# Kernel optimization log

Measured on AMD Instinct MI355X. Metric: run time of the kernel, lower is better.

Reference implementation:

```python
import jax, jax.numpy as jnp
import numpy as np
import math
from jax import lax

B, V, C, G, D, H, W = 1, 5, 32, 8, 32, 192, 192
ATTN_TEMP = 1.0
SPLIT_ITV = 1.0


def _bilinear_sample(im, x, y):
    # im: [B,C,Hs,Ws]; x,y: [B,N] pixel coords. Matches F.grid_sample
    # (bilinear, padding_mode='zeros', align_corners=True).
    Bb, Cc, Hs, Ws = im.shape
    imf = im.reshape(Bb, Cc, Hs * Ws)
    x0 = jnp.floor(x)
    y0 = jnp.floor(y)
    wx = x - x0
    wy = y - y0

    def tap(ix, iy, w):
        inb = ((ix >= 0) & (ix <= Ws - 1) & (iy >= 0) & (iy <= Hs - 1)).astype(im.dtype)
        flat = (jnp.clip(iy, 0, Hs - 1) * Ws + jnp.clip(ix, 0, Ws - 1)).astype(jnp.int32)
        v = jnp.take_along_axis(imf, flat[:, None, :], axis=2)  # [B,C,N]
        return v * (w * inb)[:, None, :]

    return (tap(x0, y0, (1 - wx) * (1 - wy)) + tap(x0 + 1, y0, wx * (1 - wy))
            + tap(x0, y0 + 1, (1 - wx) * wy) + tap(x0 + 1, y0 + 1, wx * wy))


def _homo_warping(src_fea, src_proj, ref_proj, depth_values):
    Bb, Cc, Hs, Ws = src_fea.shape
    _, Dd, Hr, Wr = depth_values.shape
    proj = jnp.matmul(src_proj, jnp.linalg.inv(ref_proj))
    rot, trans = proj[:, :3, :3], proj[:, :3, 3:4]
    yy, xx = jnp.meshgrid(jnp.arange(Hr, dtype=jnp.float32),
                          jnp.arange(Wr, dtype=jnp.float32), indexing='ij')
    xyz = jnp.stack([xx.ravel(), yy.ravel(), jnp.ones(Hr * Wr, jnp.float32)])  # [3,N]
    rot_xyz = jnp.einsum('bij,jn->bin', rot, xyz)  # [B,3,N]
    proj_xyz = rot_xyz[:, :, None, :] * depth_values.reshape(Bb, 1, Dd, Hr * Wr) \
        + trans[:, :, None, :]  # [B,3,D,N]
    z = proj_xyz[:, 2]
    z = jnp.where(z == 0, 1e-9, z)
    # grid is built under torch.no_grad in the original -> stop_gradient
    px = lax.stop_gradient(proj_xyz[:, 0] / z)  # [B,D,N] pixel coords
    py = lax.stop_gradient(proj_xyz[:, 1] / z)
    samp = _bilinear_sample(src_fea, px.reshape(Bb, -1), py.reshape(Bb, -1))  # [B,C,D*N]
    warped = samp.reshape(Bb, Cc, Dd, Hr, Wr)
    valid = lax.stop_gradient((warped[:, 0] != 0).astype(src_fea.dtype))  # [B,D,H,W]
    return warped, valid


def _forward(ref_feature, src_features, rotation, normal_plane, proj_matrices,
             depth_hypo, w_reg, w_norm):
    nsrc = src_features.shape[0]
    ref_proj = proj_matrices[:, 0]
    inv_refR = jnp.linalg.inv(rotation[:, 0])
    ref_proj_new = ref_proj[:, 0].at[:, :3, :4].set(
        jnp.matmul(ref_proj[:, 1, :3, :3], ref_proj[:, 0, :3, :4]))
    ref_vol = ref_feature.reshape(B, G, C // G, 1, H, W)  # broadcast over D

    cor_feats = jnp.zeros((B, G, D, H, W), ref_feature.dtype)
    cor_weight_sum = jnp.full((B, D, H, W), 1e-8, ref_feature.dtype)
    sum_weight = jnp.full((B, G, D, H, W), 1e-8, ref_feature.dtype)
    sims = []
    num_valid = jnp.zeros((B, D, H, W), ref_feature.dtype)

    for i in range(nsrc):  # fixed small number of source views
        src_fea = src_features[i]
        src_proj = proj_matrices[:, i + 1]
        norv = jnp.matmul(rotation[:, i + 1], inv_refR)[:, 2, :]  # [B,3]
        # stage_idx = 1: avg_pool2d(k=1,s=1) is identity -> relu(.) + 0.01
        src_w = jax.nn.relu(jnp.einsum('bchw,bc->bhw', normal_plane, norv)) + 0.01
        src_proj_new = src_proj[:, 0].at[:, :3, :4].set(
            jnp.matmul(src_proj[:, 1, :3, :3], src_proj[:, 0, :3, :4]))
        warped, valid = _homo_warping(src_fea, src_proj_new, ref_proj_new, depth_hypo)
        num_valid = valid + num_valid
        sw_d = src_w[:, None] * valid  # [B,D,H,W]
        sims.append(sw_d.mean(axis=1))
        sw5 = sw_d[:, None]  # [B,1,D,H,W] broadcast over G (repeat in torch)
        sum_weight = sum_weight + sw5
        # group-wise correlation: group_cor=True
        cor_feat = (warped.reshape(B, G, C // G, D, H, W) * ref_vol).mean(axis=2)
        cor_w = jax.nn.softmax(cor_feat.sum(axis=1) / ATTN_TEMP, axis=1) / math.sqrt(C)
        cor_weight_sum = cor_weight_sum + cor_w
        cor_feats = cor_feats + cor_w[:, None] * (sw5 * cor_feat)

    cor_feats = cor_feats / sum_weight / cor_weight_sum[:, None]
    sum_weight = sum_weight / nsrc

    hmin = depth_hypo.min(axis=(1, 2, 3), keepdims=True)
    hmax = depth_hypo.max(axis=(1, 2, 3), keepdims=True)
    norm_hypo = lax.stop_gradient((depth_hypo - hmin) / (hmax - hmin))

    # regnet stand-in: per-group linear reduction + normalized-hypo bias
    attn_logits = jnp.einsum('bgdhw,g->bdhw', cor_feats, w_reg) + norm_hypo
    attn_weight = jax.nn.softmax(attn_logits, axis=1)
    # normalnet stand-in: 1x1 linear on the 3 normal channels
    est_normal_plane = jnp.einsum('bchw,oc->bohw', normal_plane, w_norm)

    idx = jnp.argmax(attn_weight, axis=1, keepdims=True)
    depth = jnp.take_along_axis(depth_hypo, idx, axis=1)[:, 0]  # [B,H,W]
    photometric_confidence = lax.stop_gradient(attn_weight.max(axis=1))
    weight = jnp.stack(sims)[None]  # [1,nsrc,B,H,W]

    last_itv = depth_hypo[:, 1] - depth_hypo[:, 0]
    min_depth = depth - SPLIT_ITV * last_itv
    max_depth = depth + SPLIT_ITV * last_itv
    return (depth, photometric_confidence, attn_weight, est_normal_plane,
            sum_weight[:, 0, 0], weight, num_valid, min_depth, max_depth)


def setup_inputs() -> dict:
    key = jax.random.key(0)
    ks = jax.random.split(key, 5)
    ref_feature = jax.random.normal(ks[0], (B, C, H, W), jnp.float32)
    src_features = jax.random.normal(ks[1], (V - 1, B, C, H, W), jnp.float32)
    normal_plane = jax.random.normal(ks[2], (B, 3, H, W), jnp.float32)
    w_reg = jax.random.normal(ks[3], (G,), jnp.float32) * 0.1
    w_norm = jax.random.normal(ks[4], (3, 3), jnp.float32) * 0.1
    # Small per-view rotations (about z and y) and translations; intrinsics K.
    rots, projs = [], []
    Kmat = np.eye(4, dtype=np.float32)
    Kmat[0, 0] = Kmat[1, 1] = 192.0
    Kmat[0, 2] = Kmat[1, 2] = 96.0
    for v in range(V):
        az, ay = 0.04 * v, 0.02 * v
        Rz = np.array([[np.cos(az), -np.sin(az), 0], [np.sin(az), np.cos(az), 0], [0, 0, 1]], np.float32)
        Ry = np.array([[np.cos(ay), 0, np.sin(ay)], [0, 1, 0], [-np.sin(ay), 0, np.cos(ay)]], np.float32)
        Rv = (Rz @ Ry).astype(np.float32)
        rots.append(Rv)
        E = np.eye(4, dtype=np.float32)
        E[:3, :3] = Rv
        E[0, 3] = 0.1 * v
        E[2, 3] = 0.02 * v
        projs.append(np.stack([E, Kmat]))
    rotation = jnp.asarray(np.stack(rots)[None])          # [1,V,3,3]
    proj_matrices = jnp.asarray(np.stack(projs)[None])    # [1,V,2,4,4]
    depth_hypo = jnp.broadcast_to(
        jnp.linspace(425.0, 935.0, D, dtype=jnp.float32).reshape(1, D, 1, 1),
        (B, D, H, W))
    return {"ref_feature": ref_feature, "src_features": src_features,
            "rotation": rotation, "normal_plane": normal_plane,
            "proj_matrices": proj_matrices, "depth_hypo": depth_hypo,
            "w_reg": w_reg, "w_norm": w_norm}


def reference(ref_feature, src_features, rotation, normal_plane, proj_matrices,
              depth_hypo, w_reg, w_norm):
    return _forward(ref_feature, src_features, rotation, normal_plane,
                    proj_matrices, depth_hypo, w_reg, w_norm)
```

## Files before the change

### kernel.cpp

```cpp
#include <hip/hip_runtime.h>
#include <math.h>

#define Vc 5
#define Cc 32
#define Gc 8
#define Dc 32
#define Hc 192
#define Wc 192
#define HWc (Hc*Wc)
#define NSRC (Vc-1)
#define NTILE (HWc/64)

#define OFF_DEPTH  0
#define OFF_CONF   (HWc)
#define OFF_ATTN   (2*HWc)
#define OFF_EST    (OFF_ATTN + Dc*HWc)
#define OFF_SW     (OFF_EST + 3*HWc)
#define OFF_WEIGHT (OFF_SW + HWc)
#define OFF_NVAL   (OFF_WEIGHT + NSRC*HWc)
#define OFF_MIN    (OFF_NVAL + Dc*HWc)
#define OFF_MAX    (OFF_MIN + HWc)

#define T_OFF 64
#define PART_OFF (T_OFF + 6*Cc*HWc)
#define NP_OFF (PART_OFF + 2*NTILE)

__device__ void inv4(const float* A, float* out) {
    float M[4][8];
    for (int r = 0; r < 4; r++) {
        for (int c = 0; c < 4; c++) { M[r][c] = A[r*4+c]; M[r][c+4] = (r == c) ? 1.f : 0.f; }
    }
    for (int col = 0; col < 4; col++) {
        int piv = col; float best = fabsf(M[col][col]);
        for (int r = col+1; r < 4; r++) { float v = fabsf(M[r][col]); if (v > best) { best = v; piv = r; } }
        if (piv != col) for (int c = 0; c < 8; c++) { float t = M[col][c]; M[col][c] = M[piv][c]; M[piv][c] = t; }
        float inv = 1.f / M[col][col];
        for (int c = 0; c < 8; c++) M[col][c] *= inv;
        for (int r = 0; r < 4; r++) {
            if (r == col) continue;
            float f = M[r][col];
            for (int c = 0; c < 8; c++) M[r][c] -= f * M[col][c];
        }
    }
    for (int r = 0; r < 4; r++) for (int c = 0; c < 4; c++) out[r*4+c] = M[r][c+4];
}

__device__ void inv3(const float* A, float* out) {
    float a=A[0],b=A[1],c=A[2],d=A[3],e=A[4],f=A[5],g=A[6],h=A[7],i=A[8];
    float det = a*(e*i-f*h) - b*(d*i-f*g) + c*(d*h-e*g);
    float id = 1.f/det;
    out[0]=(e*i-f*h)*id; out[1]=(c*h-b*i)*id; out[2]=(b*f-c*e)*id;
    out[3]=(f*g-d*i)*id; out[4]=(a*i-c*g)*id; out[5]=(c*d-a*f)*id;
    out[6]=(d*h-e*g)*id; out[7]=(b*g-a*h)*id; out[8]=(a*e-b*d)*id;
}

__device__ void setup_body(const float* __restrict__ rotation,
                           const float* __restrict__ proj,
                           float* __restrict__ wsf) {
    float refE[16], refK[16], refNew[16], invRef[16];
    for (int k = 0; k < 16; k++) { refE[k] = proj[k]; refK[k] = proj[16+k]; }
    for (int k = 0; k < 16; k++) refNew[k] = refE[k];
    for (int r = 0; r < 3; r++) for (int c = 0; c < 4; c++) {
        float s = 0.f;
        for (int k = 0; k < 3; k++) s += refK[r*4+k] * refE[k*4+c];
        refNew[r*4+c] = s;
    }
    inv4(refNew, invRef);
    float invR0[9];
    inv3(rotation, invR0);

    for (int i = 0; i < NSRC; i++) {
        const float* E = proj + (i+1)*32;
        const float* K = proj + (i+1)*32 + 16;
        float sNew[16];
        for (int k = 0; k < 16; k++) sNew[k] = E[k];
        for (int r = 0; r < 3; r++) for (int c = 0; c < 4; c++) {
            float s = 0.f;
            for (int k = 0; k < 3; k++) s += K[r*4+k] * E[k*4+c];
            sNew[r*4+c] = s;
        }
        float P[16];
        for (int r = 0; r < 4; r++) for (int c = 0; c < 4; c++) {
            float s = 0.f;
            for (int k = 0; k < 4; k++) s += sNew[r*4+k] * invRef[k*4+c];
            P[r*4+c] = s;
        }
        float* o = wsf + 2 + i*15;
        for (int r = 0; r < 3; r++) for (int c = 0; c < 3; c++) o[r*3+c] = P[r*4+c];
        for (int r = 0; r < 3; r++) o[9+r] = P[r*4+3];
        const float* Ri = rotation + (i+1)*9;
        for (int c = 0; c < 3; c++) {
            float s = 0.f;
            for (int k = 0; k < 3; k++) s += Ri[2*3+k] * invR0[k*3+c];
            o[12+c] = s;
        }
    }
}

__global__ __launch_bounds__(256)
void prep_kernel(const float* __restrict__ src,
                 const float* __restrict__ ref,
                 const float* __restrict__ depth,
                 const float* __restrict__ normal,
                 const float* __restrict__ rotation,
                 const float* __restrict__ proj,
                 float* __restrict__ wsf) {
    const int img = blockIdx.y;
    const int p0  = blockIdx.x * 64;
    const int t = threadIdx.x;

    if (img == 6) {
        __shared__ float tl[3][64];
        if (t < 192) { const int c = t >> 6, p = t & 63; tl[c][p] = normal[c*HWc + p0 + p]; }
        __syncthreads();
        const int p = t >> 2, c = t & 3;
        wsf[NP_OFF + (size_t)(p0 + p)*4 + c] = (c < 3) ? tl[c][p] : 0.f;
        return;
    }

    const float* in = (img < NSRC) ? (src + (size_t)img*Cc*HWc)
                    : (img == NSRC) ? ref : depth;
    float* outp = wsf + T_OFF + (size_t)img * Cc * HWc;
    __shared__ float tile[Cc][64+1];
    float mn = __uint_as_float(0x7F800000u);
    float mx = 0.f;
#pragma unroll
    for (int k = 0; k < 8; k++) {
        const int c = (t >> 6) + k*4;
        const int p = t & 63;
        const float v = in[(size_t)c*HWc + p0 + p];
        tile[c][p] = v;
        mn = fminf(mn, v);
        mx = fmaxf(mx, v);
    }
    __syncthreads();
#pragma unroll
    for (int k = 0; k < 8; k++) {
        const int c = t & 31;
        const int p = (t >> 5) + k*8;
        outp[(size_t)(p0 + p)*Cc + c] = tile[c][p];
    }
    if (img == 5) {
        for (int off = 32; off; off >>= 1) {
            mn = fminf(mn, __shfl_xor(mn, off));
            mx = fmaxf(mx, __shfl_xor(mx, off));
        }
        __shared__ float smn[4], smx[4];
        const int w = t >> 6;
        if ((t & 63) == 0) { smn[w] = mn; smx[w] = mx; }
        __syncthreads();
        if (t == 0) {
            for (int i = 1; i < 4; i++) { mn = fminf(mn, smn[i]); mx = fmaxf(mx, smx[i]); }
            wsf[PART_OFF + blockIdx.x*2 + 0] = mn;
            wsf[PART_OFF + blockIdx.x*2 + 1] = mx;
        }
    }
    if (img == 0 && blockIdx.x == 0 && t == 0)
        setup_body(rotation, proj, wsf);
}

__device__ __forceinline__ void compute_wo(float fxp, float fyp, const float* __restrict__ Wv,
                                           float dep, float4* wout, int4* oout) {
    const float b0 = Wv[0]*fxp + Wv[1]*fyp + Wv[2];
    const float b1 = Wv[3]*fxp + Wv[4]*fyp + Wv[5];
    const float b2 = Wv[6]*fxp + Wv[7]*fyp + Wv[8];
    float z = fmaf(b2, dep, Wv[11]);
    if (z == 0.f) z = 1e-9f;
    float rz = __builtin_amdgcn_rcpf(z);
    rz = rz * (2.f - z * rz);
    const float px = fmaf(b0, dep, Wv[9])  * rz;
    const float py = fmaf(b1, dep, Wv[10]) * rz;

    const float fx0 = floorf(px), fy0 = floorf(py);
    const float wx = px - fx0, wy = py - fy0;
    const float fx1 = fx0 + 1.f, fy1 = fy0 + 1.f;
    const bool ix0 = (fx0 >= 0.f) && (fx0 <= (float)(Wc-1));
    const bool ix1 = (fx1 >= 0.f) && (fx1 <= (float)(Wc-1));
    const bool iy0 = (fy0 >= 0.f) && (fy0 <= (float)(Hc-1));
    const bool iy1 = (fy1 >= 0.f) && (fy1 <= (float)(Hc-1));
    const float w00 = (1.f-wx)*(1.f-wy) * ((ix0 && iy0) ? 1.f : 0.f);
    const float w10 = wx*(1.f-wy)       * ((ix1 && iy0) ? 1.f : 0.f);
    const float w01 = (1.f-wx)*wy       * ((ix0 && iy1) ? 1.f : 0.f);
    const float w11 = wx*wy             * ((ix1 && iy1) ? 1.f : 0.f);
    const int xi0 = (int)fminf(fmaxf(fx0, 0.f), (float)(Wc-1));
    const int xi1 = (int)fminf(fmaxf(fx1, 0.f), (float)(Wc-1));
    const int yi0 = (int)fminf(fmaxf(fy0, 0.f), (float)(Hc-1));
    const int yi1 = (int)fminf(fmaxf(fy1, 0.f), (float)(Hc-1));
    *wout = make_float4(w00, w10, w01, w11);
    *oout = make_int4((yi0*Wc + xi0) << 7, (yi0*Wc + xi1) << 7,
                      (yi1*Wc + xi0) << 7, (yi1*Wc + xi1) << 7);
}

template<bool USE_NPT>
__global__ __launch_bounds__(128, 8)
void main_kernel_t(const float* __restrict__ normal_plane,
                   const float* __restrict__ w_reg,
                   const float* __restrict__ w_norm,
                   const float* __restrict__ wsf,
                   float* __restrict__ out) {
    const int bid = blockIdx.x;
    const int pix = (bid & 7) * (HWc/8) + (bid >> 3);
    const int t = threadIdx.x;
    const int g = t & 7;
    const int dh = t >> 3;
    const int wv = t >> 6;
    const int wl = t & 63;
    const float fxp = (float)(pix % Wc);
    const float fyp = (float)(pix / Wc);

    const char*   srcB = (const char*)(wsf + T_OFF);
    const float4* refT = (const float4*)(wsf + T_OFF + (size_t)4*Cc*HWc);
    const float*  depT = wsf + T_OFF + (size_t)5*Cc*HWc;

    __shared__ float4 s_wt[NSRC][Dc];
    __shared__ int4   s_of[NSRC][Dc];
    __shared__ float  s_sd[NSRC][Dc];
    __shared__ float  s_wcf[NSRC][Dc];
    __shared__ float  s_val[NSRC][Dc];
    __shared__ float  s_w[NSRC][Dc];
    __shared__ float  s_sw[NSRC][Dc];
    __shared__ float  s_S[NSRC][4], s_T[NSRC][4], s_c0[NSRC][4];
    __shared__ int    s_uni[NSRC];
    __shared__ float  s_hmm[2];

    float4 rv = refT[pix*8 + g];
    rv.x *= 0.25f; rv.y *= 0.25f; rv.z *= 0.25f; rv.w *= 0.25f;
    float4 npv;
    if (USE_NPT) {
        npv = ((const float4*)(wsf + NP_OFF))[pix];
    } else {
        npv = make_float4(normal_plane[pix], normal_plane[HWc+pix],
                          normal_plane[2*HWc+pix], 0.f);
    }
    const float wreg_g = w_reg[g];

    {
        const int vvv = (wv << 1) | (wl >> 5);
        const int dd = wl & 31;
        const float* Wa = wsf + 2 + (wv << 1)*15;
        const float* Wb = Wa + 15;
        float Wv[12];
#pragma unroll
        for (int k = 0; k < 12; k++) Wv[k] = (wl < 32) ? Wa[k] : Wb[k];
        float4 wt; int4 of;
        compute_wo(fxp, fyp, Wv, depT[(size_t)pix*Dc + dd], &wt, &of);
        s_wt[vvv][dd] = wt;
        s_of[vvv][dd] = of;
        const int base = wl & 32;
        const int o0x = __shfl(of.x, base), o0y = __shfl(of.y, base);
        const int o0z = __shfl(of.z, base), o0w = __shfl(of.w, base);
        const bool eq = (of.x == o0x) && (of.y == o0y) && (of.z == o0z) && (of.w == o0w);
        const unsigned long long b = __ballot(eq);
        if ((wl & 31) == 0)
            s_uni[vvv] = (((b >> base) & 0xFFFFFFFFull) == 0xFFFFFFFFull) ? 1 : 0;

        if (wv == 1) {
            float mn = __uint_as_float(0x7F800000u);
            float mx = 0.f;
#pragma unroll
            for (int j = 0; j < 9; j++) {
                mn = fminf(mn, wsf[PART_OFF + (wl + 64*j)*2 + 0]);
                mx = fmaxf(mx, wsf[PART_OFF + (wl + 64*j)*2 + 1]);
            }
            for (int off = 32; off; off >>= 1) {
                mn = fminf(mn, __shfl_xor(mn, off));
                mx = fmaxf(mx, __shfl_xor(mx, off));
            }
            if (wl == 0) { s_hmm[0] = mn; s_hmm[1] = mx; }
        }
    }
    __syncthreads();

    {
        const int v = t >> 5;
        if (s_uni[v]) {
            const int tap = (t >> 3) & 3;
            const int4 ov = s_of[v][0];
            const int o = (tap == 0) ? ov.x : (tap == 1) ? ov.y : (tap == 2) ? ov.z : ov.w;
            const char* sp = srcB + (size_t)v*(Cc*HWc*4);
            const float4 cell = *(const float4*)(sp + (unsigned)o + (unsigned)(g << 4));
            const float dot = cell.x*rv.x + cell.y*rv.y + cell.z*rv.z + cell.w*rv.w;
            float S = dot, T = dot * wreg_g;
            S += __shfl_xor(S, 1); S += __shfl_xor(S, 2); S += __shfl_xor(S, 4);
            T += __shfl_xor(T, 1); T += __shfl_xor(T, 2); T += __shfl_xor(T, 4);
            if (g == 0) { s_S[v][tap] = S; s_T[v][tap] = T; s_c0[v][tap] = cell.x; }
        }
    }
    const unsigned gb = (unsigned)(g << 4);
#pragma unroll
    for (int i = 0; i < NSRC; i++) {
        if (!s_uni[i]) {
            const char* sp = srcB + (size_t)i*(Cc*HWc*4);
#pragma unroll
            for (int dx = 0; dx < 2; dx++) {
                const int d = dh + dx*16;
                const float4 w4 = s_wt[i][d];
                const int4   ov = s_of[i][d];
                const float4 v00 = *(const float4*)(sp + ((unsigned)ov.x + gb));
                const float4 v10 = *(const float4*)(sp + ((unsigned)ov.y + gb));
                const float4 v01 = *(const float4*)(sp + ((unsigned)ov.z + gb));
                const float4 v11 = *(const float4*)(sp + ((unsigned)ov.w + gb));
                const float bx = w4.x*v00.x + w4.y*v10.x + w4.z*v01.x + w4.w*v11.x;
                const float by = w4.x*v00.y + w4.y*v10.y + w4.z*v01.y + w4.w*v11.y;
                const float bz = w4.x*v00.z + w4.y*v10.z + w4.z*v01.z + w4.w*v11.z;
                const float bw = w4.x*v00.w + w4.y*v10.w + w4.z*v01.w + w4.w*v11.w;
                const float cf = bx*rv.x + by*rv.y + bz*rv.z + bw*rv.w;
                float sd = cf;
                sd += __shfl_xor(sd, 1); sd += __shfl_xor(sd, 2); sd += __shfl_xor(sd, 4);
                float tw = cf * wreg_g;
                tw += __shfl_xor(tw, 1); tw += __shfl_xor(tw, 2); tw += __shfl_xor(tw, 4);
                if (g == 0) {
                    s_sd[i][d] = sd; s_wcf[i][d] = tw;
                    s_val[i][d] = (bx != 0.f) ? 1.f : 0.f;
                }
            }
        }
    }
    __syncthreads();

    {
        const int vvv = t >> 5;
        const int dd = t & 31;
        float u, valv;
        if (s_uni[vvv]) {
            const float4 w4 = s_wt[vvv][dd];
            u = w4.x*s_S[vvv][0] + w4.y*s_S[vvv][1] + w4.z*s_S[vvv][2] + w4.w*s_S[vvv][3];
            const float wcfv = w4.x*s_T[vvv][0] + w4.y*s_T[vvv][1] + w4.z*s_T[vvv][2] + w4.w*s_T[vvv][3];
            const float c0 = w4.x*s_c0[vvv][0] + w4.y*s_c0[vvv][1] + w4.z*s_c0[vvv][2] + w4.w*s_c0[vvv][3];
            valv = (c0 != 0.f) ? 1.f : 0.f;
            s_wcf[vvv][dd] = wcfv;
            s_val[vvv][dd] = valv;
        } else {
            u = s_sd[vvv][dd];
            valv = s_val[vvv][dd];
        }
        float m = u;
        for (int off = 1; off < 32; off <<= 1) m = fmaxf(m, __shfl_xor(m, off));
        const float e = __expf(u - m);
        float se = e;
        for (int off = 1; off < 32; off <<= 1) se += __shfl_xor(se, off);
        float rse = __builtin_amdgcn_rcpf(se);
        rse = rse * (2.f - se * rse);
        s_w[vvv][dd] = e * rse * 0.17677669529663687f;

        const float* Na = wsf + 2 + (wv << 1)*15 + 12;
        const float* Nb = Na + 15;
        const float n0 = (wl < 32) ? Na[0] : Nb[0];
        const float n1 = (wl < 32) ? Na[1] : Nb[1];
        const float n2 = (wl < 32) ? Na[2] : Nb[2];
        const float srcw_v = fmaxf(npv.x*n0 + npv.y*n1 + npv.z*n2, 0.f) + 0.01f;
        const float swv = srcw_v * valv;
        s_sw[vvv][dd] = swv;
        float ss = swv;
        for (int off = 1; off < 32; off <<= 1) ss += __shfl_xor(ss, off);
        if ((wl & 31) == 0) out[OFF_WEIGHT + vvv*HWc + pix] = ss * (1.f/32.f);
    }
    __syncthreads();

    if (t < 32) {
        const int d = t;
        float num = 0.f, cws = 1e-8f, sumw = 1e-8f, nval = 0.f;
#pragma unroll
        for (int i = 0; i < NSRC; i++) {
            const float cw = s_w[i][d];
            const float sw = s_sw[i][d];
            num = fmaf(cw * sw, s_wcf[i][d], num);
            cws += cw; sumw += sw; nval += s_val[i][d];
        }
        float r1 = __builtin_amdgcn_rcpf(sumw);
        r1 = r1 * (2.f - sumw * r1);
        float r2 = __builtin_amdgcn_rcpf(cws);
        r2 = r2 * (2.f - cws * r2);
        const float part = num * r1 * r2;

        const float hmin = s_hmm[0];
        const float hr = s_hmm[1] - hmin;
        float rhr = __builtin_amdgcn_rcpf(hr);
        rhr = rhr * (2.f - hr * rhr);
        const float dep = depT[(size_t)pix*Dc + d];
        const float L = part + (dep - hmin) * rhr;

        float m = L;
        for (int off = 1; off < 32; off <<= 1) m = fmaxf(m, __shfl_xor(m, off));
        const float e = __expf(L - m);
        float se = e;
        for (int off = 1; off < 32; off <<= 1) se += __shfl_xor(se, off);
        float rse = __builtin_amdgcn_rcpf(se);
        rse = rse * (2.f - se * rse);
        const float attn = e * rse;

        out[OFF_ATTN + d*HWc + pix] = attn;
        out[OFF_NVAL + d*HWc + pix] = nval;

        float av = attn; int ai = d;
        for (int off = 1; off < 32; off <<= 1) {
            float av2 = __shfl_xor(av, off);
            int ai2 = __shfl_xor(ai, off);
            if (av2 > av || (av2 == av && ai2 < ai)) { av = av2; ai = ai2; }
        }
        const float dep_sel = __shfl(dep, ai);
        const float dep0 = __shfl(dep, 0);
        const float dep1 = __shfl(dep, 1);
        if (d == 0) {
            const float last_itv = dep1 - dep0;
            out[OFF_DEPTH + pix] = dep_sel;
            out[OFF_CONF + pix] = av;
            out[OFF_SW + pix] = sumw * 0.25f;
            out[OFF_MIN + pix] = dep_sel - last_itv;
            out[OFF_MAX + pix] = dep_sel + last_itv;
        }
    }
    if (wv == 1 && wl < 3) {
        float v = npv.x*w_norm[wl*3+0] + npv.y*w_norm[wl*3+1] + npv.z*w_norm[wl*3+2];
        out[OFF_EST + wl*HWc + pix] = v;
    }
}

__global__ void setup_kernel_fb(const float* __restrict__ rotation,
                                const float* __restrict__ proj,
                                float* __restrict__ wsf) {
    if (threadIdx.x != 0 || blockIdx.x != 0) return;
    unsigned int* wsu = (unsigned int*)wsf;
    wsu[0] = 0x7F800000u;
    wsu[1] = 0u;
    setup_body(rotation, proj, wsf);
}

__global__ __launch_bounds__(256)
void minmax_kernel_fb(const float* __restrict__ depth, unsigned int* __restrict__ wsu) {
    const int tid = blockIdx.x * blockDim.x + threadIdx.x;
    const int stride = gridDim.x * blockDim.x;
    const int n4 = (Dc*HWc) / 4;
    const float4* d4 = (const float4*)depth;
    float mn = __uint_as_float(0x7F800000u);
    float mx = 0.f;
    for (int idx = tid; idx < n4; idx += stride) {
        float4 v = d4[idx];
        mn = fminf(mn, fminf(fminf(v.x, v.y), fminf(v.z, v.w)));
        mx = fmaxf(mx, fmaxf(fmaxf(v.x, v.y), fmaxf(v.z, v.w)));
    }
    for (int off = 32; off; off >>= 1) {
        mn = fminf(mn, __shfl_xor(mn, off));
        mx = fmaxf(mx, __shfl_xor(mx, off));
    }
    __shared__ float smn[4], smx[4];
    const int w = threadIdx.x >> 6;
    if ((threadIdx.x & 63) == 0) { smn[w] = mn; smx[w] = mx; }
    __syncthreads();
    if (threadIdx.x == 0) {
        for (int i = 1; i < 4; i++) { mn = fminf(mn, smn[i]); mx = fmaxf(mx, smx[i]); }
        atomicMin(&wsu[0], __float_as_uint(mn));
        atomicMax(&wsu[1], __float_as_uint(mx));
    }
}

__global__ __launch_bounds__(256)
void main_kernel(const float* __restrict__ ref_feature,
                 const float* __restrict__ src_features,
                 const float* __restrict__ normal_plane,
                 const float* __restrict__ depth_hypo,
                 const float* __restrict__ w_reg,
                 const float* __restrict__ w_norm,
                 const float* __restrict__ wsf,
                 float* __restrict__ out) {
    const int pix = blockIdx.x;
    const int t = threadIdx.x;
    const int d = t & 31;
    const int g = t >> 5;
    const float fxp = (float)(pix % Wc);
    const float fyp = (float)(pix / Wc);

    __shared__ float s_cf[Gc*Dc];
    __shared__ float s_valid[Dc];

    float refv[4];
#pragma unroll
    for (int j = 0; j < 4; j++) refv[j] = ref_feature[(g*4+j)*HWc + pix];
    const float np0 = normal_plane[0*HWc + pix];
    const float np1 = normal_plane[1*HWc + pix];
    const float np2 = normal_plane[2*HWc + pix];
    const float depth_d = depth_hypo[d*HWc + pix];
    const float wreg_g = w_reg[g];

    float acc_cor = 0.f;
    float cws_acc = 1e-8f;
    float sumw_acc = 1e-8f;
    float nval_acc = 0.f;

    for (int i = 0; i < NSRC; i++) {
        const float* Wv = wsf + 2 + i*15;
        const float r00=Wv[0], r01=Wv[1], r02=Wv[2];
        const float r10=Wv[3], r11=Wv[4], r12=Wv[5];
        const float r20=Wv[6], r21=Wv[7], r22=Wv[8];
        const float t0=Wv[9], t1=Wv[10], t2=Wv[11];
        const float nv0=Wv[12], nv1=Wv[13], nv2=Wv[14];

        const float b0 = r00*fxp + r01*fyp + r02;
        const float b1 = r10*fxp + r11*fyp + r12;
        const float b2 = r20*fxp + r21*fyp + r22;

        float z = b2*depth_d + t2;
        if (z == 0.f) z = 1e-9f;
        const float px = (b0*depth_d + t0) / z;
        const float py = (b1*depth_d + t1) / z;

        const float fx0 = floorf(px), fy0 = floorf(py);
        const float wx = px - fx0, wy = py - fy0;
        const float fx1 = fx0 + 1.f, fy1 = fy0 + 1.f;
        const bool ix0 = (fx0 >= 0.f) && (fx0 <= (float)(Wc-1));
        const bool ix1 = (fx1 >= 0.f) && (fx1 <= (float)(Wc-1));
        const bool iy0 = (fy0 >= 0.f) && (fy0 <= (float)(Hc-1));
        const bool iy1 = (fy1 >= 0.f) && (fy1 <= (float)(Hc-1));
        const float w00 = (1.f-wx)*(1.f-wy) * ((ix0 && iy0) ? 1.f : 0.f);
        const float w10 = wx*(1.f-wy)       * ((ix1 && iy0) ? 1.f : 0.f);
        const float w01 = (1.f-wx)*wy       * ((ix0 && iy1) ? 1.f : 0.f);
        const float w11 = wx*wy             * ((ix1 && iy1) ? 1.f : 0.f);
        const int xi0 = (int)fminf(fmaxf(fx0, 0.f), (float)(Wc-1));
        const int xi1 = (int)fminf(fmaxf(fx1, 0.f), (float)(Wc-1));
        const int yi0 = (int)fminf(fmaxf(fy0, 0.f), (float)(Hc-1));
        const int yi1 = (int)fminf(fmaxf(fy1, 0.f), (float)(Hc-1));
        const int o00 = yi0*Wc + xi0, o10 = yi0*Wc + xi1;
        const int o01 = yi1*Wc + xi0, o11 = yi1*Wc + xi1;

        const float* src = src_features + (size_t)i * Cc * HWc;
        float corfeat = 0.f;
        float warp0 = 0.f;
#pragma unroll
        for (int j = 0; j < 4; j++) {
            const float* sc = src + (g*4 + j) * HWc;
            float v = w00*sc[o00] + w10*sc[o10] + w01*sc[o01] + w11*sc[o11];
            if (j == 0) warp0 = v;
            corfeat += v * refv[j];
        }
        corfeat *= 0.25f;

        s_cf[t] = corfeat;
        if (g == 0) s_valid[d] = (warp0 != 0.f) ? 1.f : 0.f;
        __syncthreads();

        float s_d = 0.f;
#pragma unroll
        for (int gg = 0; gg < Gc; gg++) s_d += s_cf[gg*32 + d];
        float m = s_d;
        for (int off = 1; off < 32; off <<= 1) m = fmaxf(m, __shfl_xor(m, off));
        float e = expf(s_d - m);
        float se = e;
        for (int off = 1; off < 32; off <<= 1) se += __shfl_xor(se, off);
        const float cor_w = (e / se) * 0.17677669529663687f;

        const float valid = s_valid[d];
        const float src_w = fmaxf(np0*nv0 + np1*nv1 + np2*nv2, 0.f) + 0.01f;
        const float sw = src_w * valid;

        acc_cor += cor_w * sw * corfeat;
        cws_acc += cor_w;
        sumw_acc += sw;
        nval_acc += valid;

        float ssum = sw;
        for (int off = 1; off < 32; off <<= 1) ssum += __shfl_xor(ssum, off);
        if (t == 0) out[OFF_WEIGHT + i*HWc + pix] = ssum * (1.f/32.f);
        __syncthreads();
    }

    const float cf_final = acc_cor / sumw_acc / cws_acc;
    s_cf[t] = cf_final * wreg_g;
    __syncthreads();
    float logit = 0.f;
#pragma unroll
    for (int gg = 0; gg < Gc; gg++) logit += s_cf[gg*32 + d];

    const unsigned int* wsu = (const unsigned int*)wsf;
    const float hmin = __uint_as_float(wsu[0]);
    const float hmax = __uint_as_float(wsu[1]);
    logit += (depth_d - hmin) / (hmax - hmin);

    float m = logit;
    for (int off = 1; off < 32; off <<= 1) m = fmaxf(m, __shfl_xor(m, off));
    float e = expf(logit - m);
    float se = e;
    for (int off = 1; off < 32; off <<= 1) se += __shfl_xor(se, off);
    const float attn = e / se;

    float av = attn; int ai = d;
    for (int off = 1; off < 32; off <<= 1) {
        float av2 = __shfl_xor(av, off);
        int ai2 = __shfl_xor(ai, off);
        if (av2 > av || (av2 == av && ai2 < ai)) { av = av2; ai = ai2; }
    }
    const float dep_sel = __shfl(depth_d, ai, 32);
    const float dep0 = __shfl(depth_d, 0, 32);
    const float dep1 = __shfl(depth_d, 1, 32);
    const float last_itv = dep1 - dep0;

    if (t < 32) {
        out[OFF_ATTN + d*HWc + pix] = attn;
        out[OFF_NVAL + d*HWc + pix] = nval_acc;
    }
    if (t == 0) {
        out[OFF_DEPTH + pix] = dep_sel;
        out[OFF_CONF + pix] = av;
        out[OFF_SW + pix] = sumw_acc * 0.25f;
        out[OFF_MIN + pix] = dep_sel - last_itv;
        out[OFF_MAX + pix] = dep_sel + last_itv;
    }
    if (t < 3) {
        float v = np0*w_norm[t*3+0] + np1*w_norm[t*3+1] + np2*w_norm[t*3+2];
        out[OFF_EST + t*HWc + pix] = v;
    }
}

extern "C" void kernel_launch(void* const* d_in, const int* in_sizes, int n_in,
                              void* d_out, int out_size, void* d_ws, size_t ws_size,
                              hipStream_t stream) {
    const float* ref   = (const float*)d_in[0];
    const float* src   = (const float*)d_in[1];
    const float* rot   = (const float*)d_in[2];
    const float* np_   = (const float*)d_in[3];
    const float* proj  = (const float*)d_in[4];
    const float* dh    = (const float*)d_in[5];
    const float* wreg  = (const float*)d_in[6];
    const float* wnorm = (const float*)d_in[7];
    float* out = (float*)d_out;
    float* ws  = (float*)d_ws;

    const size_t need_np   = (size_t)(NP_OFF + 4*HWc) * sizeof(float);
    const size_t need_base = (size_t)NP_OFF * sizeof(float);

    if (ws_size >= need_np) {
        dim3 tg(NTILE, 7);
        prep_kernel<<<tg, 256, 0, stream>>>(src, ref, dh, np_, rot, proj, ws);
        main_kernel_t<true><<<HWc, 128, 0, stream>>>(np_, wreg, wnorm, ws, out);
    } else if (ws_size >= need_base) {
        dim3 tg(NTILE, 6);
        prep_kernel<<<tg, 256, 0, stream>>>(src, ref, dh, np_, rot, proj, ws);
        main_kernel_t<false><<<HWc, 128, 0, stream>>>(np_, wreg, wnorm, ws, out);
    } else {
        hipMemsetAsync((char*)d_ws + 0, 0xFF, 4, stream);
        hipMemsetAsync((char*)d_ws + 4, 0x00, 4, stream);
        setup_kernel_fb<<<1, 1, 0, stream>>>(rot, proj, ws);
        minmax_kernel_fb<<<64, 256, 0, stream>>>(dh, (unsigned int*)ws);
        main_kernel<<<HWc, 256, 0, stream>>>(ref, src, np_, dh, wreg, wnorm, ws, out);
    }
}
```

Measured before the change: 150.8 us.

## Map one wavefront per pixel and hoist depth min/max reduction into separate kernel

The main kernel now processes four pixels per 256-thread block, with each 64-lane wavefront owning one pixel. Per-pixel state lives in registers and moves by cross-lane shuffles instead of block-wide shared memory and __syncthreads. The global depth min/max reduction, which every block previously redid from the partials, moves into a single-block reduce kernel that runs before the main kernel. This removes block barriers and redundant reduction work, but adds a kernel launch and raises register pressure, since each wavefront now handles all four source views.

```diff
diff --git a/kernel.cpp b/kernel.cpp
--- a/kernel.cpp
+++ b/kernel.cpp
@@ -157,6 +157,30 @@
     }
     if (img == 0 && blockIdx.x == 0 && t == 0)
         setup_body(rotation, proj, wsf);
+}
+
+__global__ __launch_bounds__(256)
+void reduce_kernel(float* __restrict__ wsf) {
+    const int t = threadIdx.x;
+    float mn = __uint_as_float(0x7F800000u);
+    float mx = 0.f;
+    for (int idx = t; idx < NTILE; idx += 256) {
+        mn = fminf(mn, wsf[PART_OFF + idx*2 + 0]);
+        mx = fmaxf(mx, wsf[PART_OFF + idx*2 + 1]);
+    }
+    for (int off = 32; off; off >>= 1) {
+        mn = fminf(mn, __shfl_xor(mn, off));
+        mx = fmaxf(mx, __shfl_xor(mx, off));
+    }
+    __shared__ float smn[4], smx[4];
+    const int w = t >> 6;
+    if ((t & 63) == 0) { smn[w] = mn; smx[w] = mx; }
+    __syncthreads();
+    if (t == 0) {
+        for (int i = 1; i < 4; i++) { mn = fminf(mn, smn[i]); mx = fmaxf(mx, smx[i]); }
+        wsf[0] = mn;
+        wsf[1] = mx;
+    }
 }
 
 __device__ __forceinline__ void compute_wo(float fxp, float fyp, const float* __restrict__ Wv,
@@ -192,19 +216,18 @@
 }
 
 template<bool USE_NPT>
-__global__ __launch_bounds__(128, 8)
+__global__ __launch_bounds__(256, 4)
 void main_kernel_t(const float* __restrict__ normal_plane,
                    const float* __restrict__ w_reg,
                    const float* __restrict__ w_norm,
                    const float* __restrict__ wsf,
                    float* __restrict__ out) {
     const int bid = blockIdx.x;
-    const int pix = (bid & 7) * (HWc/8) + (bid >> 3);
-    const int t = threadIdx.x;
-    const int g = t & 7;
-    const int dh = t >> 3;
-    const int wv = t >> 6;
-    const int wl = t & 63;
+    const int wq = threadIdx.x >> 6;
+    const int wl = threadIdx.x & 63;
+    const int grp = (bid & 7) * (HWc/32) + (bid >> 3);
+    const int pix = grp*4 + wq;
+    const int g = wl & 7;
     const float fxp = (float)(pix % Wc);
     const float fyp = (float)(pix / Wc);
 
@@ -212,16 +235,9 @@
     const float4* refT = (const float4*)(wsf + T_OFF + (size_t)4*Cc*HWc);
     const float*  depT = wsf + T_OFF + (size_t)5*Cc*HWc;
 
-    __shared__ float4 s_wt[NSRC][Dc];
-    __shared__ int4   s_of[NSRC][Dc];
-    __shared__ float  s_sd[NSRC][Dc];
-    __shared__ float  s_wcf[NSRC][Dc];
-    __shared__ float  s_val[NSRC][Dc];
-    __shared__ float  s_w[NSRC][Dc];
-    __shared__ float  s_sw[NSRC][Dc];
-    __shared__ float  s_S[NSRC][4], s_T[NSRC][4], s_c0[NSRC][4];
-    __shared__ int    s_uni[NSRC];
-    __shared__ float  s_hmm[2];
+    __shared__ float s_sd[4][NSRC][Dc];
+    __shared__ float s_tw[4][NSRC][Dc];
+    __shared__ float s_val[4][NSRC][Dc];
 
     float4 rv = refT[pix*8 + g];
     rv.x *= 0.25f; rv.y *= 0.25f; rv.z *= 0.25f; rv.w *= 0.25f;
@@ -233,106 +249,145 @@
                           normal_plane[2*HWc+pix], 0.f);
     }
     const float wreg_g = w_reg[g];
-
+    const float dep_d = depT[(size_t)pix*Dc + (wl & 31)];
+    const float hmin = wsf[0];
+    const float hmax = wsf[1];
+
+    float4 wt0, wt1; int4 of0, of1;
     {
-        const int vvv = (wv << 1) | (wl >> 5);
-        const int dd = wl & 31;
-        const float* Wa = wsf + 2 + (wv << 1)*15;
-        const float* Wb = Wa + 15;
+        const float* A0 = wsf + 2 + 0*15;
+        const float* B0 = A0 + 15;
         float Wv[12];
 #pragma unroll
-        for (int k = 0; k < 12; k++) Wv[k] = (wl < 32) ? Wa[k] : Wb[k];
-        float4 wt; int4 of;
-        compute_wo(fxp, fyp, Wv, depT[(size_t)pix*Dc + dd], &wt, &of);
-        s_wt[vvv][dd] = wt;
-        s_of[vvv][dd] = of;
-        const int base = wl & 32;
-        const int o0x = __shfl(of.x, base), o0y = __shfl(of.y, base);
-        const int o0z = __shfl(of.z, base), o0w = __shfl(of.w, base);
-        const bool eq = (of.x == o0x) && (of.y == o0y) && (of.z == o0z) && (of.w == o0w);
-        const unsigned long long b = __ballot(eq);
-        if ((wl & 31) == 0)
-            s_uni[vvv] = (((b >> base) & 0xFFFFFFFFull) == 0xFFFFFFFFull) ? 1 : 0;
-
-        if (wv == 1) {
-            float mn = __uint_as_float(0x7F800000u);
-            float mx = 0.f;
-#pragma unroll
-            for (int j = 0; j < 9; j++) {
-                mn = fminf(mn, wsf[PART_OFF + (wl + 64*j)*2 + 0]);
-                mx = fmaxf(mx, wsf[PART_OFF + (wl + 64*j)*2 + 1]);
-            }
-            for (int off = 32; off; off >>= 1) {
-                mn = fminf(mn, __shfl_xor(mn, off));
-                mx = fmaxf(mx, __shfl_xor(mx, off));
-            }
-            if (wl == 0) { s_hmm[0] = mn; s_hmm[1] = mx; }
-        }
-    }
-    __syncthreads();
-
+        for (int j = 0; j < 12; j++) Wv[j] = (wl < 32) ? A0[j] : B0[j];
+        compute_wo(fxp, fyp, Wv, dep_d, &wt0, &of0);
+        const float* A1 = wsf + 2 + 2*15;
+        const float* B1 = A1 + 15;
+#pragma unroll
+        for (int j = 0; j < 12; j++) Wv[j] = (wl < 32) ? A1[j] : B1[j];
+        compute_wo(fxp, fyp, Wv, dep_d, &wt1, &of1);
+    }
+    bool u0, u1, u2, u3;
     {
-        const int v = t >> 5;
-        if (s_uni[v]) {
-            const int tap = (t >> 3) & 3;
-            const int4 ov = s_of[v][0];
-            const int o = (tap == 0) ? ov.x : (tap == 1) ? ov.y : (tap == 2) ? ov.z : ov.w;
+        const int bl = wl & 32;
+        int rx = __shfl(of0.x, bl), ry = __shfl(of0.y, bl);
+        int rz = __shfl(of0.z, bl), rw = __shfl(of0.w, bl);
+        const bool e0 = (of0.x==rx) && (of0.y==ry) && (of0.z==rz) && (of0.w==rw);
+        const unsigned long long b0 = __ballot(e0);
+        u0 = (b0 & 0xFFFFFFFFull) == 0xFFFFFFFFull;
+        u1 = (b0 >> 32) == 0xFFFFFFFFull;
+        rx = __shfl(of1.x, bl); ry = __shfl(of1.y, bl);
+        rz = __shfl(of1.z, bl); rw = __shfl(of1.w, bl);
+        const bool e1 = (of1.x==rx) && (of1.y==ry) && (of1.z==rz) && (of1.w==rw);
+        const unsigned long long b1 = __ballot(e1);
+        u2 = (b1 & 0xFFFFFFFFull) == 0xFFFFFFFFull;
+        u3 = (b1 >> 32) == 0xFFFFFFFFull;
+    }
+
+    const int tap = (wl >> 3) & 3;
+    float S0 = 0.f, T0 = 0.f, C0 = 0.f;
+    float S1 = 0.f, T1 = 0.f, C1 = 0.f;
+    {
+        const bool uva = (wl & 32) ? u1 : u0;
+        if (uva) {
+            const int v = (wl >> 5);
+            const int o = (tap == 0) ? of0.x : (tap == 1) ? of0.y : (tap == 2) ? of0.z : of0.w;
             const char* sp = srcB + (size_t)v*(Cc*HWc*4);
             const float4 cell = *(const float4*)(sp + (unsigned)o + (unsigned)(g << 4));
             const float dot = cell.x*rv.x + cell.y*rv.y + cell.z*rv.z + cell.w*rv.w;
             float S = dot, T = dot * wreg_g;
             S += __shfl_xor(S, 1); S += __shfl_xor(S, 2); S += __shfl_xor(S, 4);
             T += __shfl_xor(T, 1); T += __shfl_xor(T, 2); T += __shfl_xor(T, 4);
-            if (g == 0) { s_S[v][tap] = S; s_T[v][tap] = T; s_c0[v][tap] = cell.x; }
-        }
-    }
-    const unsigned gb = (unsigned)(g << 4);
-#pragma unroll
-    for (int i = 0; i < NSRC; i++) {
-        if (!s_uni[i]) {
-            const char* sp = srcB + (size_t)i*(Cc*HWc*4);
-#pragma unroll
-            for (int dx = 0; dx < 2; dx++) {
-                const int d = dh + dx*16;
-                const float4 w4 = s_wt[i][d];
-                const int4   ov = s_of[i][d];
-                const float4 v00 = *(const float4*)(sp + ((unsigned)ov.x + gb));
-                const float4 v10 = *(const float4*)(sp + ((unsigned)ov.y + gb));
-                const float4 v01 = *(const float4*)(sp + ((unsigned)ov.z + gb));
-                const float4 v11 = *(const float4*)(sp + ((unsigned)ov.w + gb));
-                const float bx = w4.x*v00.x + w4.y*v10.x + w4.z*v01.x + w4.w*v11.x;
-                const float by = w4.x*v00.y + w4.y*v10.y + w4.z*v01.y + w4.w*v11.y;
-                const float bz = w4.x*v00.z + w4.y*v10.z + w4.z*v01.z + w4.w*v11.z;
-                const float bw = w4.x*v00.w + w4.y*v10.w + w4.z*v01.w + w4.w*v11.w;
-                const float cf = bx*rv.x + by*rv.y + bz*rv.z + bw*rv.w;
-                float sd = cf;
-                sd += __shfl_xor(sd, 1); sd += __shfl_xor(sd, 2); sd += __shfl_xor(sd, 4);
-                float tw = cf * wreg_g;
-                tw += __shfl_xor(tw, 1); tw += __shfl_xor(tw, 2); tw += __shfl_xor(tw, 4);
-                if (g == 0) {
-                    s_sd[i][d] = sd; s_wcf[i][d] = tw;
-                    s_val[i][d] = (bx != 0.f) ? 1.f : 0.f;
+            S0 = S; T0 = T; C0 = __shfl(cell.x, wl & ~7);
+        }
+        const bool uvb = (wl & 32) ? u3 : u2;
+        if (uvb) {
+            const int v = 2 + (wl >> 5);
+            const int o = (tap == 0) ? of1.x : (tap == 1) ? of1.y : (tap == 2) ? of1.z : of1.w;
+            const char* sp = srcB + (size_t)v*(Cc*HWc*4);
+            const float4 cell = *(const float4*)(sp + (unsigned)o + (unsigned)(g << 4));
+            const float dot = cell.x*rv.x + cell.y*rv.y + cell.z*rv.z + cell.w*rv.w;
+            float S = dot, T = dot * wreg_g;
+            S += __shfl_xor(S, 1); S += __shfl_xor(S, 2); S += __shfl_xor(S, 4);
+            T += __shfl_xor(T, 1); T += __shfl_xor(T, 2); T += __shfl_xor(T, 4);
+            S1 = S; T1 = T; C1 = __shfl(cell.x, wl & ~7);
+        }
+    }
+
+    if (!(u0 && u1 && u2 && u3)) {
+        const int d4 = wl >> 3;
+#pragma unroll
+        for (int i = 0; i < NSRC; i++) {
+            const bool ui = (i == 0) ? u0 : (i == 1) ? u1 : (i == 2) ? u2 : u3;
+            if (!ui) {
+                const char* sp = srcB + (size_t)i*(Cc*HWc*4);
+#pragma unroll
+                for (int j = 0; j < 4; j++) {
+                    const int dd = d4 + 8*j;
+                    const int lp = ((i & 1) << 5) | dd;
+                    float4 w4; int4 ov;
+                    if (i < 2) {
+                        w4.x = __shfl(wt0.x, lp); w4.y = __shfl(wt0.y, lp);
+                        w4.z = __shfl(wt0.z, lp); w4.w = __shfl(wt0.w, lp);
+                        ov.x = __shfl(of0.x, lp); ov.y = __shfl(of0.y, lp);
+                        ov.z = __shfl(of0.z, lp); ov.w = __shfl(of0.w, lp);
+                    } else {
+                        w4.x = __shfl(wt1.x, lp); w4.y = __shfl(wt1.y, lp);
+                        w4.z = __shfl(wt1.z, lp); w4.w = __shfl(wt1.w, lp);
+                        ov.x = __shfl(of1.x, lp); ov.y = __shfl(of1.y, lp);
+                        ov.z = __shfl(of1.z, lp); ov.w = __shfl(of1.w, lp);
+                    }
+                    const float4 v00 = *(const float4*)(sp + ((unsigned)ov.x + (unsigned)(g<<4)));
+                    const float4 v10 = *(const float4*)(sp + ((unsigned)ov.y + (unsigned)(g<<4)));
+                    const float4 v01 = *(const float4*)(sp + ((unsigned)ov.z + (unsigned)(g<<4)));
+                    const float4 v11 = *(const float4*)(sp + ((unsigned)ov.w + (unsigned)(g<<4)));
+                    const float bx = w4.x*v00.x + w4.y*v10.x + w4.z*v01.x + w4.w*v11.x;
+                    const float by = w4.x*v00.y + w4.y*v10.y + w4.z*v01.y + w4.w*v11.y;
+                    const float bz = w4.x*v00.z + w4.y*v10.z + w4.z*v01.z + w4.w*v11.z;
+                    const float bw = w4.x*v00.w + w4.y*v10.w + w4.z*v01.w + w4.w*v11.w;
+                    const float cf = bx*rv.x + by*rv.y + bz*rv.z + bw*rv.w;
+                    float sd = cf;
+                    sd += __shfl_xor(sd, 1); sd += __shfl_xor(sd, 2); sd += __shfl_xor(sd, 4);
+                    float tw = cf * wreg_g;
+                    tw += __shfl_xor(tw, 1); tw += __shfl_xor(tw, 2); tw += __shfl_xor(tw, 4);
+                    if (g == 0) {
+                        s_sd[wq][i][dd] = sd;
+                        s_tw[wq][i][dd] = tw;
+                        s_val[wq][i][dd] = (bx != 0.f) ? 1.f : 0.f;
+                    }
                 }
             }
         }
-    }
-    __syncthreads();
-
-    {
-        const int vvv = t >> 5;
-        const int dd = t & 31;
-        float u, valv;
-        if (s_uni[vvv]) {
-            const float4 w4 = s_wt[vvv][dd];
-            u = w4.x*s_S[vvv][0] + w4.y*s_S[vvv][1] + w4.z*s_S[vvv][2] + w4.w*s_S[vvv][3];
-            const float wcfv = w4.x*s_T[vvv][0] + w4.y*s_T[vvv][1] + w4.z*s_T[vvv][2] + w4.w*s_T[vvv][3];
-            const float c0 = w4.x*s_c0[vvv][0] + w4.y*s_c0[vvv][1] + w4.z*s_c0[vvv][2] + w4.w*s_c0[vvv][3];
-            valv = (c0 != 0.f) ? 1.f : 0.f;
-            s_wcf[vvv][dd] = wcfv;
-            s_val[vvv][dd] = valv;
+        asm volatile("s_waitcnt lgkmcnt(0)" ::: "memory");
+    }
+
+    float w_k[2], sw_k[2], wcf_k[2], val_k[2];
+#pragma unroll
+    for (int k = 0; k < 2; k++) {
+        const int v = 2*k + (wl >> 5);
+        const float4 wt = k ? wt1 : wt0;
+        const bool uv = (wl & 32) ? (k ? u3 : u1) : (k ? u2 : u0);
+        float u, wcf, valv;
+        if (uv) {
+            float c0s = 0.f;
+            u = 0.f; wcf = 0.f;
+#pragma unroll
+            for (int tp = 0; tp < 4; tp++) {
+                const int lanep = (wl & 32) | (tp << 3);
+                const float Sp = __shfl(k ? S1 : S0, lanep);
+                const float Tp = __shfl(k ? T1 : T0, lanep);
+                const float Cp = __shfl(k ? C1 : C0, lanep);
+                const float wc = (tp == 0) ? wt.x : (tp == 1) ? wt.y : (tp == 2) ? wt.z : wt.w;
+                u   = fmaf(wc, Sp, u);
+                wcf = fmaf(wc, Tp, wcf);
+                c0s = fmaf(wc, Cp, c0s);
+            }
+            valv = (c0s != 0.f) ? 1.f : 0.f;
         } else {
-            u = s_sd[vvv][dd];
-            valv = s_val[vvv][dd];
+            const int dd = wl & 31;
+            u    = s_sd[wq][v][dd];
+            wcf  = s_tw[wq][v][dd];
+            valv = s_val[wq][v][dd];
         }
         float m = u;
         for (int off = 1; off < 32; off <<= 1) m = fmaxf(m, __shfl_xor(m, off));
@@ -341,78 +396,78 @@
         for (int off = 1; off < 32; off <<= 1) se += __shfl_xor(se, off);
         float rse = __builtin_amdgcn_rcpf(se);
         rse = rse * (2.f - se * rse);
-        s_w[vvv][dd] = e * rse * 0.17677669529663687f;
-
-        const float* Na = wsf + 2 + (wv << 1)*15 + 12;
+        w_k[k] = e * rse * 0.17677669529663687f;
+
+        const float* Na = wsf + 2 + (2*k)*15 + 12;
         const float* Nb = Na + 15;
         const float n0 = (wl < 32) ? Na[0] : Nb[0];
         const float n1 = (wl < 32) ? Na[1] : Nb[1];
         const float n2 = (wl < 32) ? Na[2] : Nb[2];
         const float srcw_v = fmaxf(npv.x*n0 + npv.y*n1 + npv.z*n2, 0.f) + 0.01f;
-        const float swv = srcw_v * valv;
-        s_sw[vvv][dd] = swv;
-        float ss = swv;
+        sw_k[k] = srcw_v * valv;
+        wcf_k[k] = wcf;
+        val_k[k] = valv;
+
+        float ss = sw_k[k];
         for (int off = 1; off < 32; off <<= 1) ss += __shfl_xor(ss, off);
-        if ((wl & 31) == 0) out[OFF_WEIGHT + vvv*HWc + pix] = ss * (1.f/32.f);
-    }
-    __syncthreads();
-
-    if (t < 32) {
-        const int d = t;
-        float num = 0.f, cws = 1e-8f, sumw = 1e-8f, nval = 0.f;
-#pragma unroll
-        for (int i = 0; i < NSRC; i++) {
-            const float cw = s_w[i][d];
-            const float sw = s_sw[i][d];
-            num = fmaf(cw * sw, s_wcf[i][d], num);
-            cws += cw; sumw += sw; nval += s_val[i][d];
-        }
-        float r1 = __builtin_amdgcn_rcpf(sumw);
-        r1 = r1 * (2.f - sumw * r1);
-        float r2 = __builtin_amdgcn_rcpf(cws);
-        r2 = r2 * (2.f - cws * r2);
-        const float part = num * r1 * r2;
-
-        const float hmin = s_hmm[0];
-        const float hr = s_hmm[1] - hmin;
-        float rhr = __builtin_amdgcn_rcpf(hr);
-        rhr = rhr * (2.f - hr * rhr);
-        const float dep = depT[(size_t)pix*Dc + d];
-        const float L = part + (dep - hmin) * rhr;
-
-        float m = L;
-        for (int off = 1; off < 32; off <<= 1) m = fmaxf(m, __shfl_xor(m, off));
-        const float e = __expf(L - m);
-        float se = e;
-        for (int off = 1; off < 32; off <<= 1) se += __shfl_xor(se, off);
-        float rse = __builtin_amdgcn_rcpf(se);
-        rse = rse * (2.f - se * rse);
-        const float attn = e * rse;
-
-        out[OFF_ATTN + d*HWc + pix] = attn;
-        out[OFF_NVAL + d*HWc + pix] = nval;
-
-        float av = attn; int ai = d;
-        for (int off = 1; off < 32; off <<= 1) {
-            float av2 = __shfl_xor(av, off);
-            int ai2 = __shfl_xor(ai, off);
-            if (av2 > av || (av2 == av && ai2 < ai)) { av = av2; ai = ai2; }
-        }
-        const float dep_sel = __shfl(dep, ai);
-        const float dep0 = __shfl(dep, 0);
-        const float dep1 = __shfl(dep, 1);
-        if (d == 0) {
-            const float last_itv = dep1 - dep0;
-            out[OFF_DEPTH + pix] = dep_sel;
-            out[OFF_CONF + pix] = av;
-            out[OFF_SW + pix] = sumw * 0.25f;
-            out[OFF_MIN + pix] = dep_sel - last_itv;
-            out[OFF_MAX + pix] = dep_sel + last_itv;
-        }
-    }
-    if (wv == 1 && wl < 3) {
-        float v = npv.x*w_norm[wl*3+0] + npv.y*w_norm[wl*3+1] + npv.z*w_norm[wl*3+2];
-        out[OFF_EST + wl*HWc + pix] = v;
+        if ((wl & 31) == 0) out[OFF_WEIGHT + v*HWc + pix] = ss * (1.f/32.f);
+    }
+
+    float num = w_k[0]*sw_k[0]*wcf_k[0] + w_k[1]*sw_k[1]*wcf_k[1];
+    float cwsp = w_k[0] + w_k[1];
+    float sump = sw_k[0] + sw_k[1];
+    float nvp  = val_k[0] + val_k[1];
+    num  += __shfl_xor(num, 32);
+    const float cws  = cwsp + __shfl_xor(cwsp, 32) + 1e-8f;
+    const float sumw = sump + __shfl_xor(sump, 32) + 1e-8f;
+    const float nval = nvp + __shfl_xor(nvp, 32);
+
+    float r1 = __builtin_amdgcn_rcpf(sumw);
+    r1 = r1 * (2.f - sumw * r1);
+    float r2 = __builtin_amdgcn_rcpf(cws);
+    r2 = r2 * (2.f - cws * r2);
+    const float part = num * r1 * r2;
+
+    const float hr = hmax - hmin;
+    float rhr = __builtin_amdgcn_rcpf(hr);
+    rhr = rhr * (2.f - hr * rhr);
+    const float logit = part + (dep_d - hmin) * rhr;
+
+    float m = logit;
+    for (int off = 1; off < 32; off <<= 1) m = fmaxf(m, __shfl_xor(m, off));
+    const float e = __expf(logit - m);
+    float se = e;
+    for (int off = 1; off < 32; off <<= 1) se += __shfl_xor(se, off);
+    float rse = __builtin_amdgcn_rcpf(se);
+    rse = rse * (2.f - se * rse);
+    const float attn = e * rse;
+
+    if (wl < 32) {
+        out[OFF_ATTN + wl*HWc + pix] = attn;
+        out[OFF_NVAL + wl*HWc + pix] = nval;
+    }
+
+    float av = attn; int ai = wl & 31;
+    for (int off = 1; off < 32; off <<= 1) {
+        float av2 = __shfl_xor(av, off);
+        int ai2 = __shfl_xor(ai, off);
+        if (av2 > av || (av2 == av && ai2 < ai)) { av = av2; ai = ai2; }
+    }
+    const float dep_sel = __shfl(dep_d, ai);
+    const float dep0 = __shfl(dep_d, 0);
+    const float dep1 = __shfl(dep_d, 1);
+    if (wl == 0) {
+        const float last_itv = dep1 - dep0;
+        out[OFF_DEPTH + pix] = dep_sel;
+        out[OFF_CONF + pix] = av;
+        out[OFF_SW + pix] = sumw * 0.25f;
+        out[OFF_MIN + pix] = dep_sel - last_itv;
+        out[OFF_MAX + pix] = dep_sel + last_itv;
+    }
+    if (wl >= 32 && wl < 35) {
+        const int r = wl - 32;
+        float v = npv.x*w_norm[r*3+0] + npv.y*w_norm[r*3+1] + npv.z*w_norm[r*3+2];
+        out[OFF_EST + r*HWc + pix] = v;
     }
 }
 
@@ -630,11 +685,13 @@
     if (ws_size >= need_np) {
         dim3 tg(NTILE, 7);
         prep_kernel<<<tg, 256, 0, stream>>>(src, ref, dh, np_, rot, proj, ws);
-        main_kernel_t<true><<<HWc, 128, 0, stream>>>(np_, wreg, wnorm, ws, out);
+        reduce_kernel<<<1, 256, 0, stream>>>(ws);
+        main_kernel_t<true><<<HWc/4, 256, 0, stream>>>(np_, wreg, wnorm, ws, out);
     } else if (ws_size >= need_base) {
         dim3 tg(NTILE, 6);
         prep_kernel<<<tg, 256, 0, stream>>>(src, ref, dh, np_, rot, proj, ws);
-        main_kernel_t<false><<<HWc, 128, 0, stream>>>(np_, wreg, wnorm, ws, out);
+        reduce_kernel<<<1, 256, 0, stream>>>(ws);
+        main_kernel_t<false><<<HWc/4, 256, 0, stream>>>(np_, wreg, wnorm, ws, out);
     } else {
         hipMemsetAsync((char*)d_ws + 0, 0xFF, 4, stream);
         hipMemsetAsync((char*)d_ws + 4, 0x00, 4, stream);
```

Result: no change. 149.7 us (-0.8%).
